# Performance work log

Hardware: AMD Instinct MI355X
Metric: run time of the kernel (lower is better)

The kernel has to match this reference:

```python
import jax, jax.numpy as jnp
import numpy as np

N_NODES = 14   # input_size: nodes of the graph
SEQ = 24       # seq_len == GAT in/out feature dim == output_size
GAT_HID = 64
MLP_HID = 64
NEG_SLOPE = 0.2  # PyG GATConv default leaky_relu slope
B = 32768
N_EDGES = 56


def setup_inputs() -> dict:
    key = jax.random.key(0)
    ks = jax.random.split(key, 16)
    def w(k, shape, fan_in):
        return jax.random.normal(k, shape, dtype=jnp.float32) / np.sqrt(fan_in)
    return {
        "x": jax.random.normal(ks[0], (B, SEQ, N_NODES), dtype=jnp.float32),
        "edge_index": jax.random.randint(ks[1], (2, N_EDGES), 0, N_NODES, dtype=jnp.int64),
        # GATConv 1: in=24 -> out=64, heads=1
        "W1": w(ks[2], (SEQ, GAT_HID), SEQ),
        "a_src1": w(ks[3], (GAT_HID,), GAT_HID),
        "a_dst1": w(ks[4], (GAT_HID,), GAT_HID),
        "b1": jnp.zeros((GAT_HID,), dtype=jnp.float32),
        # GATConv 2: in=64 -> out=24, heads=1
        "W2": w(ks[5], (GAT_HID, SEQ), GAT_HID),
        "a_src2": w(ks[6], (SEQ,), SEQ),
        "a_dst2": w(ks[7], (SEQ,), SEQ),
        "b2": jnp.zeros((SEQ,), dtype=jnp.float32),
        # per-node 2-layer MLPs (one Linear(24,64)+ReLU+Linear(64,24) per node)
        "fc1_w": w(ks[8], (N_NODES, SEQ, MLP_HID), SEQ),
        "fc1_b": jnp.zeros((N_NODES, MLP_HID), dtype=jnp.float32),
        "fc2_w": w(ks[9], (N_NODES, MLP_HID, SEQ), MLP_HID),
        "fc2_b": jnp.zeros((N_NODES, SEQ), dtype=jnp.float32),
    }


def _gat_conv(x, src, dst, W, a_s, a_d, b):
    # PyG GATConv, heads=1, concat=False: linear -> edge attention -> edge softmax over dst -> scatter-sum
    h = x @ W                                             # [N, F]
    alpha = jax.nn.leaky_relu(h[src] @ a_s + h[dst] @ a_d, NEG_SLOPE)  # [E]
    m = jax.ops.segment_max(alpha, dst, num_segments=N_NODES)
    e = jnp.exp(alpha - m[dst])
    s = jax.ops.segment_sum(e, dst, num_segments=N_NODES)
    w = e / s[dst]
    return jax.ops.segment_sum(h[src] * w[:, None], dst, num_segments=N_NODES) + b


def reference(x, edge_index, W1, a_src1, a_dst1, b1, W2, a_src2, a_dst2, b2,
              fc1_w, fc1_b, fc2_w, fc2_b):
    ei = edge_index.astype(jnp.int32)
    loops = jnp.arange(N_NODES, dtype=jnp.int32)  # add_self_loops=True (PyG default)
    src = jnp.concatenate([ei[0], loops])
    dst = jnp.concatenate([ei[1], loops])

    def gat(xs):  # xs: [N_NODES, SEQ]
        h = jax.nn.elu(_gat_conv(xs, src, dst, W1, a_src1, a_dst1, b1))
        return _gat_conv(h, src, dst, W2, a_src2, a_dst2, b2)

    # x: [B, SEQ, N_NODES] -> transpose(1,2) -> per-sample GAT, vmapped over batch
    g = jax.vmap(gat)(x.transpose(0, 2, 1))              # [B, N_NODES, SEQ]
    # per-node 2-layer MLP, batched over nodes via einsum
    h = jax.nn.relu(jnp.einsum('bnf,nfh->bnh', g, fc1_w) + fc1_b)
    pred = jnp.einsum('bnh,nho->bno', h, fc2_w) + fc2_b  # [B, N_NODES, SEQ]
    return pred.transpose(1, 0, 2)                       # [N_NODES, B, SEQ]
```

## Files before the change

### kernel.cpp

```cpp
#include <hip/hip_runtime.h>

typedef unsigned int uu32;

#define NN 14
#define FD 24
#define HD 64
#define NE 70
#define BB 32768
#define SPW 4
#define WPB 4
#define K1_BLOCKS (BB / (WPB * SPW))
#define R2 2
#define K2_BLOCKS (NN * (BB / (256 * R2)))
#define HAP 68
#define H2P 28
#define PSZ 224

#define WSYNC() asm volatile("s_waitcnt lgkmcnt(0)" ::: "memory")

__global__ __launch_bounds__(256) void gat_k(
    const float* __restrict__ x, const int* __restrict__ ei,
    const float* __restrict__ W1, const float* __restrict__ as1,
    const float* __restrict__ ad1, const float* __restrict__ b1,
    const float* __restrict__ W2, const float* __restrict__ as2,
    const float* __restrict__ ad2, const float* __restrict__ b2,
    float* __restrict__ Gout) {
    __shared__ __align__(16) float HA[WPB][NN * HAP];
    __shared__ __align__(16) float H2S[WPB][NN * H2P];
    __shared__ __align__(16) float PS[WPB][PSZ];
    __shared__ float sdS[WPB][2 * NN];
    __shared__ float smS[WPB][NN];
    __shared__ __align__(16) float a1S[2 * HD];
    __shared__ __align__(16) float a2S[2 * FD];
    __shared__ int esS[NE], edS[NE];

    const int tid = threadIdx.x;
    const int wv = tid >> 6;
    const int lane = tid & 63;
    float* HAw = HA[wv];
    float* H2w = H2S[wv];
    float* Pw = PS[wv];
    float* sdw = sdS[wv];
    float* smw = smS[wv];

    if (tid < 2 * HD) a1S[tid] = (tid < HD) ? as1[tid] : ad1[tid - HD];
    if (tid < 2 * FD) a2S[tid] = (tid < FD) ? as2[tid] : ad2[tid - FD];
    if (tid < 56) {
        int e64 = 1;
        for (int i = 0; i < 8; i++)
            if (ei[2 * i + 1] != 0 || (uu32)ei[2 * i] >= (uu32)NN) e64 = 0;
        esS[tid] = e64 ? ei[2 * tid] : ei[tid];
        edS[tid] = e64 ? ei[112 + 2 * tid] : ei[56 + tid];
    } else if (tid < NE) {
        esS[tid] = tid - 56;
        edS[tid] = tid - 56;
    }

    float w1r[FD];
#pragma unroll
    for (int f = 0; f < FD; f++) w1r[f] = W1[f * HD + lane];
    const float b1r = b1[lane];
    const int f2 = lane % FD;
    const int g2 = lane / FD;
    float w2r[HD];
#pragma unroll
    for (int k = 0; k < HD; k++) w2r[k] = W2[k * FD + f2];
    const float b2r = b2[f2];
    __syncthreads();
    const bool ex = (lane < NE - 64);
    const int s0 = esS[lane], d0 = edS[lane];
    const int s1 = esS[ex ? 64 + lane : 0], d1 = edS[ex ? 64 + lane : 0];

    const int gw = blockIdx.x * WPB + wv;
    for (int t = 0; t < SPW; t++) {
        const int b = gw * SPW + t;
        const int bo = __builtin_amdgcn_readfirstlane(b * (NN * FD));
        const float* __restrict__ xb = x + bo;
        float acc[NN];
#pragma unroll
        for (int n = 0; n < NN; n++) acc[n] = 0.0f;
#pragma unroll
        for (int f = 0; f < FD; f++) {
            const float wf = w1r[f];
#pragma unroll
            for (int n = 0; n < NN; n++)
                acc[n] = fmaf(xb[f * NN + n], wf, acc[n]);
        }
#pragma unroll
        for (int n = 0; n < NN; n++) HAw[n * HAP + lane] = acc[n];
        WSYNC();
        if (lane < 2 * NN) {
            const int v = (lane >= NN) ? 1 : 0;
            const int n2 = lane - v * NN;
            float s = 0.0f;
#pragma unroll
            for (int k = 0; k < 16; k++) {
                float4 h4 = *(const float4*)&HAw[n2 * HAP + 4 * k];
                float4 a4 = *(const float4*)&a1S[v * HD + 4 * k];
                s = fmaf(h4.x, a4.x, s); s = fmaf(h4.y, a4.y, s);
                s = fmaf(h4.z, a4.z, s); s = fmaf(h4.w, a4.w, s);
            }
            sdw[v * NN + n2] = s;
        }
        if (lane < PSZ / 4)
            *(float4*)&Pw[lane * 4] = make_float4(0.f, 0.f, 0.f, 0.f);
        if (lane < NN) smw[lane] = 0.0f;
        WSYNC();
        {
            float a = sdw[s0] + sdw[NN + d0];
            a = a > 0.0f ? a : 0.2f * a;
            float e0 = __expf(a);
            atomicAdd(&smw[d0], e0);
            atomicAdd(&Pw[d0 * 16 + s0], e0);
            if (ex) {
                a = sdw[s1] + sdw[NN + d1];
                a = a > 0.0f ? a : 0.2f * a;
                float e1 = __expf(a);
                atomicAdd(&smw[d1], e1);
                atomicAdd(&Pw[d1 * 16 + s1], e1);
            }
        }
        WSYNC();
        float acc2[NN];
#pragma unroll
        for (int n = 0; n < NN; n++) {
            float a = 0.0f;
#pragma unroll
            for (int k4 = 0; k4 < 3; k4++) {
                float4 p4 = *(const float4*)&Pw[n * 16 + 4 * k4];
                a = fmaf(p4.x, acc[4 * k4 + 0], a);
                a = fmaf(p4.y, acc[4 * k4 + 1], a);
                a = fmaf(p4.z, acc[4 * k4 + 2], a);
                a = fmaf(p4.w, acc[4 * k4 + 3], a);
            }
            float4 p4 = *(const float4*)&Pw[n * 16 + 12];
            a = fmaf(p4.x, acc[12], a);
            a = fmaf(p4.y, acc[13], a);
            a = __fdividef(a, smw[n]) + b1r;
            acc2[n] = a > 0.0f ? a : (__expf(a) - 1.0f);
        }
#pragma unroll
        for (int n = 0; n < NN; n++) HAw[n * HAP + lane] = acc2[n];
        WSYNC();
        if (g2 < 2) {
#pragma unroll
            for (int i = 0; i < 7; i++) {
                const int n = g2 + 2 * i;
                float a = 0.0f;
#pragma unroll
                for (int k4 = 0; k4 < 16; k4++) {
                    float4 v4 = *(const float4*)&HAw[n * HAP + 4 * k4];
                    a = fmaf(v4.x, w2r[4 * k4 + 0], a);
                    a = fmaf(v4.y, w2r[4 * k4 + 1], a);
                    a = fmaf(v4.z, w2r[4 * k4 + 2], a);
                    a = fmaf(v4.w, w2r[4 * k4 + 3], a);
                }
                H2w[n * H2P + f2] = a;
            }
        }
        WSYNC();
        if (lane < 2 * NN) {
            const int v = (lane >= NN) ? 1 : 0;
            const int n2 = lane - v * NN;
            float s = 0.0f;
#pragma unroll
            for (int q = 0; q < 6; q++) {
                float4 h4 = *(const float4*)&H2w[n2 * H2P + 4 * q];
                float4 a4 = *(const float4*)&a2S[v * FD + 4 * q];
                s = fmaf(h4.x, a4.x, s); s = fmaf(h4.y, a4.y, s);
                s = fmaf(h4.z, a4.z, s); s = fmaf(h4.w, a4.w, s);
            }
            sdw[v * NN + n2] = s;
        }
        if (lane < PSZ / 4)
            *(float4*)&Pw[lane * 4] = make_float4(0.f, 0.f, 0.f, 0.f);
        if (lane < NN) smw[lane] = 0.0f;
        WSYNC();
        {
            float a = sdw[s0] + sdw[NN + d0];
            a = a > 0.0f ? a : 0.2f * a;
            float e0 = __expf(a);
            atomicAdd(&smw[d0], e0);
            atomicAdd(&Pw[d0 * 16 + s0], e0);
            if (ex) {
                a = sdw[s1] + sdw[NN + d1];
                a = a > 0.0f ? a : 0.2f * a;
                float e1 = __expf(a);
                atomicAdd(&smw[d1], e1);
                atomicAdd(&Pw[d1 * 16 + s1], e1);
            }
        }
        WSYNC();
        if (g2 < 2) {
            float h2c[NN];
#pragma unroll
            for (int k = 0; k < NN; k++) h2c[k] = H2w[k * H2P + f2];
#pragma unroll
            for (int i = 0; i < 7; i++) {
                const int n = g2 + 2 * i;
                float a = 0.0f;
#pragma unroll
                for (int k4 = 0; k4 < 3; k4++) {
                    float4 p4 = *(const float4*)&Pw[n * 16 + 4 * k4];
                    a = fmaf(p4.x, h2c[4 * k4 + 0], a);
                    a = fmaf(p4.y, h2c[4 * k4 + 1], a);
                    a = fmaf(p4.z, h2c[4 * k4 + 2], a);
                    a = fmaf(p4.w, h2c[4 * k4 + 3], a);
                }
                float4 p4 = *(const float4*)&Pw[n * 16 + 12];
                a = fmaf(p4.x, h2c[12], a);
                a = fmaf(p4.y, h2c[13], a);
                Gout[((size_t)n * BB + b) * FD + f2] =
                    __fdividef(a, smw[n]) + b2r;
            }
        }
        WSYNC();
    }
}

__global__ __launch_bounds__(256) void mlp_k(
    const float* __restrict__ fc1w, const float* __restrict__ fc1b,
    const float* __restrict__ fc2w, const float* __restrict__ fc2b,
    float* __restrict__ gio) {
    __shared__ __align__(16) float W1L[FD * HD];
    __shared__ __align__(16) float W2L[HD * FD];
    __shared__ float B1L[HD];
    __shared__ float B2L[FD];

    const int t = threadIdx.x;
    const int n = blockIdx.x >> 6;
    const int b0 = (blockIdx.x & 63) * 512;

    const float4* w1p = (const float4*)(fc1w + (size_t)n * (FD * HD));
    const float4* w2p = (const float4*)(fc2w + (size_t)n * (HD * FD));
    for (int i = t; i < 384; i += 256) {
        *(float4*)&W1L[4 * i] = w1p[i];
        *(float4*)&W2L[4 * i] = w2p[i];
    }
    if (t < HD) B1L[t] = fc1b[n * HD + t];
    if (t < FD) B2L[t] = fc2b[n * FD + t];
    __syncthreads();

    const size_t base0 = ((size_t)n * BB + b0 + t) * FD;
    const size_t base1 = base0 + (size_t)256 * FD;
    float g0[FD], g1[FD], o0[FD], o1[FD];
#pragma unroll
    for (int q = 0; q < 6; q++) {
        *(float4*)&g0[4 * q] = *(const float4*)&gio[base0 + 4 * q];
        *(float4*)&g1[4 * q] = *(const float4*)&gio[base1 + 4 * q];
    }
#pragma unroll
    for (int f = 0; f < FD; f++) { o0[f] = B2L[f]; o1[f] = o0[f]; }

#pragma unroll 1
    for (int j4 = 0; j4 < 16; j4++) {
        float h00 = B1L[4 * j4 + 0], h01 = B1L[4 * j4 + 1];
        float h02 = B1L[4 * j4 + 2], h03 = B1L[4 * j4 + 3];
        float h10 = h00, h11 = h01, h12 = h02, h13 = h03;
#pragma unroll
        for (int f = 0; f < FD; f++) {
            float4 w4 = *(const float4*)&W1L[f * HD + 4 * j4];
            h00 = fmaf(g0[f], w4.x, h00); h01 = fmaf(g0[f], w4.y, h01);
            h02 = fmaf(g0[f], w4.z, h02); h03 = fmaf(g0[f], w4.w, h03);
            h10 = fmaf(g1[f], w4.x, h10); h11 = fmaf(g1[f], w4.y, h11);
            h12 = fmaf(g1[f], w4.z, h12); h13 = fmaf(g1[f], w4.w, h13);
        }
        h00 = fmaxf(h00, 0.f); h01 = fmaxf(h01, 0.f);
        h02 = fmaxf(h02, 0.f); h03 = fmaxf(h03, 0.f);
        h10 = fmaxf(h10, 0.f); h11 = fmaxf(h11, 0.f);
        h12 = fmaxf(h12, 0.f); h13 = fmaxf(h13, 0.f);
        float hv0[4] = {h00, h01, h02, h03};
        float hv1[4] = {h10, h11, h12, h13};
#pragma unroll
        for (int u2 = 0; u2 < 4; u2++) {
            const int j = 4 * j4 + u2;
#pragma unroll
            for (int f4 = 0; f4 < 6; f4++) {
                float4 w4 = *(const float4*)&W2L[j * FD + 4 * f4];
                o0[4 * f4 + 0] = fmaf(hv0[u2], w4.x, o0[4 * f4 + 0]);
                o0[4 * f4 + 1] = fmaf(hv0[u2], w4.y, o0[4 * f4 + 1]);
                o0[4 * f4 + 2] = fmaf(hv0[u2], w4.z, o0[4 * f4 + 2]);
                o0[4 * f4 + 3] = fmaf(hv0[u2], w4.w, o0[4 * f4 + 3]);
                o1[4 * f4 + 0] = fmaf(hv1[u2], w4.x, o1[4 * f4 + 0]);
                o1[4 * f4 + 1] = fmaf(hv1[u2], w4.y, o1[4 * f4 + 1]);
                o1[4 * f4 + 2] = fmaf(hv1[u2], w4.z, o1[4 * f4 + 2]);
                o1[4 * f4 + 3] = fmaf(hv1[u2], w4.w, o1[4 * f4 + 3]);
            }
        }
    }
#pragma unroll
    for (int q = 0; q < 6; q++) {
        *(float4*)&gio[base0 + 4 * q] = *(const float4*)&o0[4 * q];
        *(float4*)&gio[base1 + 4 * q] = *(const float4*)&o1[4 * q];
    }
}

extern "C" void kernel_launch(void* const* d_in, const int* in_sizes, int n_in,
                              void* d_out, int out_size, void* d_ws, size_t ws_size,
                              hipStream_t stream) {
    (void)in_sizes; (void)n_in; (void)out_size; (void)d_ws; (void)ws_size;
    const float* x    = (const float*)d_in[0];
    const int*   ei   = (const int*)d_in[1];
    const float* W1   = (const float*)d_in[2];
    const float* as1  = (const float*)d_in[3];
    const float* ad1  = (const float*)d_in[4];
    const float* b1   = (const float*)d_in[5];
    const float* W2   = (const float*)d_in[6];
    const float* as2  = (const float*)d_in[7];
    const float* ad2  = (const float*)d_in[8];
    const float* b2   = (const float*)d_in[9];
    const float* fc1w = (const float*)d_in[10];
    const float* fc1b = (const float*)d_in[11];
    const float* fc2w = (const float*)d_in[12];
    const float* fc2b = (const float*)d_in[13];
    float* gio = (float*)d_out;

    gat_k<<<dim3(K1_BLOCKS), dim3(256), 0, stream>>>(
        x, ei, W1, as1, ad1, b1, W2, as2, ad2, b2, gio);
    mlp_k<<<dim3(K2_BLOCKS), dim3(256), 0, stream>>>(
        fc1w, fc1b, fc2w, fc2b, gio);
}
```

Baseline: 369.2 us.

## Broadcast weights and inputs via cross-lane readlane instead of LDS and global reads

The MLP kernel no longer stages per-node weights and biases in shared memory. Each lane holds one column of the weights in registers, and values are broadcast with readlane inside the inner loops. In the GAT kernel, x is loaded coalesced into six registers per lane and broadcast with readlane, and the attention matrix P and the softmax sums are also read through readlane. The H2P padding shrinks from 28 to 24. This removes LDS traffic and barriers, but adds a readlane (a VALU op writing an SGPR) for roughly every two FMAs in the MLP. That risks an instruction-issue bottleneck and readlane hazard stalls.

```diff
diff --git a/kernel.cpp b/kernel.cpp
--- a/kernel.cpp
+++ b/kernel.cpp
@@ -13,10 +13,17 @@
 #define R2 2
 #define K2_BLOCKS (NN * (BB / (256 * R2)))
 #define HAP 68
-#define H2P 28
+#define H2P 24
 #define PSZ 224
 
 #define WSYNC() asm volatile("s_waitcnt lgkmcnt(0)" ::: "memory")
+
+__device__ __forceinline__ float rdl(float v, int l) {
+    union { float f; int i; } u;
+    u.f = v;
+    u.i = __builtin_amdgcn_readlane(u.i, l);
+    return u.f;
+}
 
 __global__ __launch_bounds__(256) void gat_k(
     const float* __restrict__ x, const int* __restrict__ ei,
@@ -72,19 +79,27 @@
     const int s1 = esS[ex ? 64 + lane : 0], d1 = edS[ex ? 64 + lane : 0];
 
     const int gw = blockIdx.x * WPB + wv;
+#pragma unroll 1
     for (int t = 0; t < SPW; t++) {
-        const int b = gw * SPW + t;
-        const int bo = __builtin_amdgcn_readfirstlane(b * (NN * FD));
-        const float* __restrict__ xb = x + bo;
+        const size_t b = (size_t)gw * SPW + t;
+        const float* __restrict__ xb = x + b * (NN * FD);
+        float xr[6];
+        xr[0] = xb[lane];
+        xr[1] = xb[64 + lane];
+        xr[2] = xb[128 + lane];
+        xr[3] = xb[192 + lane];
+        xr[4] = xb[256 + lane];
+        xr[5] = (lane < NN * FD - 320) ? xb[320 + lane] : 0.0f;
         float acc[NN];
 #pragma unroll
         for (int n = 0; n < NN; n++) acc[n] = 0.0f;
 #pragma unroll
         for (int f = 0; f < FD; f++) {
-            const float wf = w1r[f];
-#pragma unroll
-            for (int n = 0; n < NN; n++)
-                acc[n] = fmaf(xb[f * NN + n], wf, acc[n]);
+#pragma unroll
+            for (int n = 0; n < NN; n++) {
+                const int i = f * NN + n;
+                acc[n] = fmaf(rdl(xr[i >> 6], i & 63), w1r[f], acc[n]);
+            }
         }
 #pragma unroll
         for (int n = 0; n < NN; n++) HAw[n * HAP + lane] = acc[n];
@@ -121,22 +136,25 @@
             }
         }
         WSYNC();
+        const float pr0 = Pw[lane];
+        const float pr1 = Pw[64 + lane];
+        const float pr2 = Pw[128 + lane];
+        const float pr3 = (lane < PSZ - 192) ? Pw[192 + lane] : 0.0f;
+        const float smr = (lane < NN) ? smw[lane] : 1.0f;
         float acc2[NN];
 #pragma unroll
         for (int n = 0; n < NN; n++) {
             float a = 0.0f;
 #pragma unroll
-            for (int k4 = 0; k4 < 3; k4++) {
-                float4 p4 = *(const float4*)&Pw[n * 16 + 4 * k4];
-                a = fmaf(p4.x, acc[4 * k4 + 0], a);
-                a = fmaf(p4.y, acc[4 * k4 + 1], a);
-                a = fmaf(p4.z, acc[4 * k4 + 2], a);
-                a = fmaf(p4.w, acc[4 * k4 + 3], a);
-            }
-            float4 p4 = *(const float4*)&Pw[n * 16 + 12];
-            a = fmaf(p4.x, acc[12], a);
-            a = fmaf(p4.y, acc[13], a);
-            a = __fdividef(a, smw[n]) + b1r;
+            for (int k = 0; k < NN; k++) {
+                const int i = n * 16 + k;
+                const float pv = (i < 64) ? rdl(pr0, i) :
+                                 (i < 128) ? rdl(pr1, i - 64) :
+                                 (i < 192) ? rdl(pr2, i - 128) :
+                                             rdl(pr3, i - 192);
+                a = fmaf(pv, acc[k], a);
+            }
+            a = __fdividef(a, rdl(smr, n)) + b1r;
             acc2[n] = a > 0.0f ? a : (__expf(a) - 1.0f);
         }
 #pragma unroll
@@ -222,24 +240,21 @@
     const float* __restrict__ fc1w, const float* __restrict__ fc1b,
     const float* __restrict__ fc2w, const float* __restrict__ fc2b,
     float* __restrict__ gio) {
-    __shared__ __align__(16) float W1L[FD * HD];
-    __shared__ __align__(16) float W2L[HD * FD];
-    __shared__ float B1L[HD];
-    __shared__ float B2L[FD];
-
     const int t = threadIdx.x;
+    const int lane = t & 63;
     const int n = blockIdx.x >> 6;
     const int b0 = (blockIdx.x & 63) * 512;
 
-    const float4* w1p = (const float4*)(fc1w + (size_t)n * (FD * HD));
-    const float4* w2p = (const float4*)(fc2w + (size_t)n * (HD * FD));
-    for (int i = t; i < 384; i += 256) {
-        *(float4*)&W1L[4 * i] = w1p[i];
-        *(float4*)&W2L[4 * i] = w2p[i];
-    }
-    if (t < HD) B1L[t] = fc1b[n * HD + t];
-    if (t < FD) B2L[t] = fc2b[n * FD + t];
-    __syncthreads();
+    const float* __restrict__ W1n = fc1w + (size_t)n * (FD * HD);
+    const float* __restrict__ W2n = fc2w + (size_t)n * (HD * FD);
+
+    float w1c[FD], w2r[FD];
+#pragma unroll
+    for (int f = 0; f < FD; f++) w1c[f] = W1n[f * HD + lane];
+#pragma unroll
+    for (int f = 0; f < FD; f++) w2r[f] = W2n[lane * FD + f];
+    const float b1r = fc1b[(size_t)n * HD + lane];
+    const float b2r = (lane < FD) ? fc2b[(size_t)n * FD + lane] : 0.0f;
 
     const size_t base0 = ((size_t)n * BB + b0 + t) * FD;
     const size_t base1 = base0 + (size_t)256 * FD;
@@ -250,41 +265,42 @@
         *(float4*)&g1[4 * q] = *(const float4*)&gio[base1 + 4 * q];
     }
 #pragma unroll
-    for (int f = 0; f < FD; f++) { o0[f] = B2L[f]; o1[f] = o0[f]; }
+    for (int f = 0; f < FD; f++) {
+        const float bv = rdl(b2r, f);
+        o0[f] = bv; o1[f] = bv;
+    }
 
 #pragma unroll 1
     for (int j4 = 0; j4 < 16; j4++) {
-        float h00 = B1L[4 * j4 + 0], h01 = B1L[4 * j4 + 1];
-        float h02 = B1L[4 * j4 + 2], h03 = B1L[4 * j4 + 3];
-        float h10 = h00, h11 = h01, h12 = h02, h13 = h03;
+        float h0[4], h1[4];
+#pragma unroll
+        for (int u = 0; u < 4; u++) {
+            const float bv = rdl(b1r, 4 * j4 + u);
+            h0[u] = bv; h1[u] = bv;
+        }
 #pragma unroll
         for (int f = 0; f < FD; f++) {
-            float4 w4 = *(const float4*)&W1L[f * HD + 4 * j4];
-            h00 = fmaf(g0[f], w4.x, h00); h01 = fmaf(g0[f], w4.y, h01);
-            h02 = fmaf(g0[f], w4.z, h02); h03 = fmaf(g0[f], w4.w, h03);
-            h10 = fmaf(g1[f], w4.x, h10); h11 = fmaf(g1[f], w4.y, h11);
-            h12 = fmaf(g1[f], w4.z, h12); h13 = fmaf(g1[f], w4.w, h13);
-        }
-        h00 = fmaxf(h00, 0.f); h01 = fmaxf(h01, 0.f);
-        h02 = fmaxf(h02, 0.f); h03 = fmaxf(h03, 0.f);
-        h10 = fmaxf(h10, 0.f); h11 = fmaxf(h11, 0.f);
-        h12 = fmaxf(h12, 0.f); h13 = fmaxf(h13, 0.f);
-        float hv0[4] = {h00, h01, h02, h03};
-        float hv1[4] = {h10, h11, h12, h13};
-#pragma unroll
-        for (int u2 = 0; u2 < 4; u2++) {
-            const int j = 4 * j4 + u2;
-#pragma unroll
-            for (int f4 = 0; f4 < 6; f4++) {
-                float4 w4 = *(const float4*)&W2L[j * FD + 4 * f4];
-                o0[4 * f4 + 0] = fmaf(hv0[u2], w4.x, o0[4 * f4 + 0]);
-                o0[4 * f4 + 1] = fmaf(hv0[u2], w4.y, o0[4 * f4 + 1]);
-                o0[4 * f4 + 2] = fmaf(hv0[u2], w4.z, o0[4 * f4 + 2]);
-                o0[4 * f4 + 3] = fmaf(hv0[u2], w4.w, o0[4 * f4 + 3]);
-                o1[4 * f4 + 0] = fmaf(hv1[u2], w4.x, o1[4 * f4 + 0]);
-                o1[4 * f4 + 1] = fmaf(hv1[u2], w4.y, o1[4 * f4 + 1]);
-                o1[4 * f4 + 2] = fmaf(hv1[u2], w4.z, o1[4 * f4 + 2]);
-                o1[4 * f4 + 3] = fmaf(hv1[u2], w4.w, o1[4 * f4 + 3]);
+            const float gf0 = g0[f], gf1 = g1[f];
+#pragma unroll
+            for (int u = 0; u < 4; u++) {
+                const float w = rdl(w1c[f], 4 * j4 + u);
+                h0[u] = fmaf(gf0, w, h0[u]);
+                h1[u] = fmaf(gf1, w, h1[u]);
+            }
+        }
+#pragma unroll
+        for (int u = 0; u < 4; u++) {
+            h0[u] = fmaxf(h0[u], 0.f);
+            h1[u] = fmaxf(h1[u], 0.f);
+        }
+#pragma unroll
+        for (int u = 0; u < 4; u++) {
+            const float a0 = h0[u], a1 = h1[u];
+#pragma unroll
+            for (int f = 0; f < FD; f++) {
+                const float w = rdl(w2r[f], 4 * j4 + u);
+                o0[f] = fmaf(a0, w, o0[f]);
+                o1[f] = fmaf(a1, w, o1[f]);
             }
         }
     }
```

After: 367.9 us. Within noise of the previous version (-0.4%).
